# Optimization experiments

Hardware: AMD Instinct MI355X
Metric: run time of the kernel (lower is better)

The kernel has to match this reference:

```python
import jax, jax.numpy as jnp
import numpy as np


def setup_inputs() -> dict:
    key = jax.random.key(0)
    k1, k2 = jax.random.split(key)
    inputs = jax.random.normal(k1, (64, 16, 64, 512), dtype=jnp.float32)
    cluster_centers = jax.random.normal(k2, (64, 512), dtype=jnp.float32) * 0.05
    return {"inputs": inputs, "cluster_centers": cluster_centers}


def reference(inputs, cluster_centers):
    # inputs: (B, H, W, C); cluster_centers: (K, C)
    B, H, W, C = inputs.shape
    K = cluster_centers.shape[0]
    x = inputs.reshape(B, H * W, C)                      # (B, N, C)
    # soft assignments: softmax over K of x @ centers^T
    logits = jnp.einsum('bnc,kc->bnk', x, cluster_centers)
    a = jax.nn.softmax(logits, axis=-1)                  # (B, N, K)
    # VLAD rewritten to avoid (B,N,K,C) residual tensor:
    # sum_n a[b,n,k] * (x[b,n,:] - c[k,:])
    #   = (a^T @ x)[b,k,:] - (sum_n a[b,n,k]) * c[k,:]
    agg = jnp.einsum('bnk,bnc->bkc', a, x)               # (B, K, C)
    a_sum = jnp.sum(a, axis=1)                           # (B, K)
    vlad = agg - a_sum[:, :, None] * cluster_centers[None, :, :]
    vlad = vlad.reshape(B, K * C)
    # tf.nn.l2_normalize: x / sqrt(max(sum(x^2), eps)), eps=1e-12
    norm = jnp.sqrt(jnp.maximum(jnp.sum(vlad * vlad, axis=-1, keepdims=True), 1e-12))
    return vlad / norm
```

## Files before the change

kernel.cpp:

```cpp
#include <hip/hip_runtime.h>
#include <stdint.h>

#define NB 64
#define NN 1024
#define CDIM 512
#define KK 64

typedef __attribute__((ext_vector_type(4))) float f32x4;
typedef __attribute__((ext_vector_type(8))) short short8;

__device__ __forceinline__ unsigned short f2bf(float f) {
  unsigned int u = __float_as_uint(f);
  return (unsigned short)((u + 0x7fffu + ((u >> 16) & 1u)) >> 16);
}
__device__ __forceinline__ float bf2f(unsigned short h) {
  return __uint_as_float(((unsigned int)h) << 16);
}

__device__ __forceinline__ void lgkm_barrier() {
  asm volatile("s_waitcnt lgkmcnt(0)" ::: "memory");
  __builtin_amdgcn_sched_barrier(0);
  __builtin_amdgcn_s_barrier();
}

__global__ __launch_bounds__(256) void k0_cvt(const float* __restrict__ cc,
                                              unsigned short* __restrict__ ccb) {
  int i = blockIdx.x * 256 + threadIdx.x;
  ccb[i] = f2bf(cc[i]);
}

__global__ __launch_bounds__(256, 1) void k1_assign(const float* __restrict__ x,
    const unsigned short* __restrict__ ccb, unsigned int* __restrict__ a_t32,
    unsigned int* __restrict__ xT32) {
  const int b = blockIdx.y;
  const int tid = threadIdx.x;
  const int w = tid >> 6;
  const int l = tid & 63;
  const int lr = l & 15;
  const int lg = l >> 4;
  const int nc = (blockIdx.x << 2) + w;
  const int n0 = nc << 6;
  const int codd = l & 1;

  __shared__ unsigned int xsw_all[4][32 * 33];
  __shared__ unsigned int asw_all[4][64 * 33];
  unsigned int* xsw = xsw_all[w];
  unsigned int* asw = asw_all[w];

  const float* xr = x + ((size_t)b * NN + n0 + lr) * CDIM + (lg << 3);
  const unsigned short* cb = ccb + lr * CDIM + (lg << 3);
  const size_t xTbase = ((size_t)((b << 4) + nc)) << 14;
  const size_t atbase = ((size_t)((b << 4) + nc)) << 11;

  f32x4 acc[4][4];
  #pragma unroll
  for (int i = 0; i < 4; ++i)
    #pragma unroll
    for (int j = 0; j < 4; ++j) acc[i][j] = (f32x4){0.f, 0.f, 0.f, 0.f};

  #pragma unroll 2
  for (int step = 0; step < 16; ++step) {
    const int cs = step << 5;
    short8 af[4];
    #pragma unroll
    for (int tn = 0; tn < 4; ++tn) {
      f32x4 xa = *(const f32x4*)(xr + (size_t)(tn << 4) * CDIM + cs);
      f32x4 xb = *(const f32x4*)(xr + (size_t)(tn << 4) * CDIM + cs + 4);
      short8 t;
      t[0] = (short)f2bf(xa[0]); t[1] = (short)f2bf(xa[1]);
      t[2] = (short)f2bf(xa[2]); t[3] = (short)f2bf(xa[3]);
      t[4] = (short)f2bf(xb[0]); t[5] = (short)f2bf(xb[1]);
      t[6] = (short)f2bf(xb[2]); t[7] = (short)f2bf(xb[3]);
      af[tn] = t;
    }
    short8 bq0 = *(const short8*)(cb + cs);
    short8 bq1 = *(const short8*)(cb + 16 * CDIM + cs);
    short8 bq2 = *(const short8*)(cb + 32 * CDIM + cs);
    short8 bq3 = *(const short8*)(cb + 48 * CDIM + cs);
    #pragma unroll
    for (int tn = 0; tn < 4; ++tn) {
      acc[tn][0] = __builtin_amdgcn_mfma_f32_16x16x32_bf16(af[tn], bq0, acc[tn][0], 0, 0, 0);
      acc[tn][1] = __builtin_amdgcn_mfma_f32_16x16x32_bf16(af[tn], bq1, acc[tn][1], 0, 0, 0);
      acc[tn][2] = __builtin_amdgcn_mfma_f32_16x16x32_bf16(af[tn], bq2, acc[tn][2], 0, 0, 0);
      acc[tn][3] = __builtin_amdgcn_mfma_f32_16x16x32_bf16(af[tn], bq3, acc[tn][3], 0, 0, 0);
    }
    #pragma unroll
    for (int tn = 0; tn < 4; ++tn) {
      #pragma unroll
      for (int q = 0; q < 4; ++q) {
        unsigned int own = ((const unsigned int*)&af[tn])[q];
        unsigned int oth = (unsigned int)__shfl_xor((int)own, 1);
        unsigned int v = codd ? ((oth >> 16) | (own & 0xffff0000u))
                              : ((own & 0xffffu) | (oth << 16));
        xsw[((lg << 3) + (q << 1) + codd) * 33 + (tn << 3) + (lr >> 1)] = v;
      }
    }
    #pragma unroll
    for (int i = 0; i < 16; ++i) {
      const int row = (i << 1) + (l >> 5);
      xT32[xTbase + ((size_t)(cs + row) << 5) + (l & 31)] = xsw[row * 33 + (l & 31)];
    }
  }

  #pragma unroll
  for (int tn = 0; tn < 4; ++tn) {
    #pragma unroll
    for (int j = 0; j < 4; ++j) {
      float m = fmaxf(fmaxf(acc[tn][0][j], acc[tn][1][j]),
                      fmaxf(acc[tn][2][j], acc[tn][3][j]));
      m = fmaxf(m, __shfl_xor(m, 1));
      m = fmaxf(m, __shfl_xor(m, 2));
      m = fmaxf(m, __shfl_xor(m, 4));
      m = fmaxf(m, __shfl_xor(m, 8));
      float e0 = __expf(acc[tn][0][j] - m);
      float e1 = __expf(acc[tn][1][j] - m);
      float e2 = __expf(acc[tn][2][j] - m);
      float e3 = __expf(acc[tn][3][j] - m);
      float s = e0 + e1 + e2 + e3;
      s += __shfl_xor(s, 1); s += __shfl_xor(s, 2);
      s += __shfl_xor(s, 4); s += __shfl_xor(s, 8);
      float inv = 1.0f / s;
      acc[tn][0][j] = e0 * inv;
      acc[tn][1][j] = e1 * inv;
      acc[tn][2][j] = e2 * inv;
      acc[tn][3][j] = e3 * inv;
    }
  }
  #pragma unroll
  for (int tn = 0; tn < 4; ++tn)
    #pragma unroll
    for (int tk = 0; tk < 4; ++tk)
      #pragma unroll
      for (int jp = 0; jp < 2; ++jp) {
        unsigned int v = (unsigned int)f2bf(acc[tn][tk][2 * jp]) |
                         ((unsigned int)f2bf(acc[tn][tk][2 * jp + 1]) << 16);
        asw[((tk << 4) + lr) * 33 + (tn << 3) + (lg << 1) + jp] = v;
      }
  #pragma unroll
  for (int i = 0; i < 32; ++i) {
    const int k = (i << 1) + (l >> 5);
    a_t32[atbase + ((size_t)k << 5) + (l & 31)] = asw[k * 33 + (l & 31)];
  }
}

#define XRS 38
__global__ __launch_bounds__(256) void k2_agg(
    const unsigned short* __restrict__ a_t, const unsigned int* __restrict__ xT32,
    const float* __restrict__ cc, float* __restrict__ out,
    float* __restrict__ sumsq) {
  const int b = blockIdx.y;
  const int c0 = blockIdx.x << 6;
  const int tid = threadIdx.x;
  const int w = tid >> 6;
  const int l = tid & 63;
  const int lr = l & 15;
  const int lg = l >> 4;

  __shared__ unsigned int xs[2][64 * XRS];
  __shared__ float red[4];

  f32x4 acc[4];
  #pragma unroll
  for (int i = 0; i < 4; ++i) acc[i] = (f32x4){0.f, 0.f, 0.f, 0.f};
  float ssum = 0.f;

  const unsigned short* ap =
      a_t + (((size_t)(b << 4)) << 12) + (((w << 4) + lr) << 6) + (lg << 3);
  const unsigned int* xg =
      xT32 + (((size_t)(b << 4)) << 14) + ((c0 + (tid >> 5)) << 5) + (tid & 31);

  #pragma unroll
  for (int p = 0; p < 8; ++p) {
    const int f = (p << 8) + tid;
    xs[0][(f >> 5) * XRS + (f & 31)] = xg[p << 8];
  }
  short8 a_cur0 = *(const short8*)(ap);
  short8 a_cur1 = *(const short8*)(ap + 32);
  lgkm_barrier();

  for (int it = 0; it < 16; ++it) {
    const int cur = it & 1;
    unsigned int xr[8];
    short8 a_nxt0, a_nxt1;
    if (it < 15) {
      const size_t cho = ((size_t)(it + 1)) << 14;
      const size_t cha = ((size_t)(it + 1)) << 12;
      #pragma unroll
      for (int p = 0; p < 8; ++p) xr[p] = xg[cho + (p << 8)];
      a_nxt0 = *(const short8*)(ap + cha);
      a_nxt1 = *(const short8*)(ap + cha + 32);
    }
    #pragma unroll
    for (int i = 0; i < 8; ++i)
      ssum += bf2f((unsigned short)a_cur0[i]) + bf2f((unsigned short)a_cur1[i]);
    #pragma unroll
    for (int ns = 0; ns < 64; ns += 32) {
      const short8 af = ns == 0 ? a_cur0 : a_cur1;
      #pragma unroll
      for (int ct = 0; ct < 4; ++ct) {
        const int row = (ct << 4) + lr;
        const unsigned long long* bp = (const unsigned long long*)
            &xs[cur][row * XRS + (ns >> 1) + (lg << 2)];
        union { unsigned long long q[2]; short8 s; } u;
        u.q[0] = bp[0];
        u.q[1] = bp[1];
        acc[ct] = __builtin_amdgcn_mfma_f32_16x16x32_bf16(af, u.s, acc[ct], 0, 0, 0);
      }
    }
    if (it < 15) {
      #pragma unroll
      for (int p = 0; p < 8; ++p) {
        const int f = (p << 8) + tid;
        xs[cur ^ 1][(f >> 5) * XRS + (f & 31)] = xr[p];
      }
      a_cur0 = a_nxt0;
      a_cur1 = a_nxt1;
    }
    lgkm_barrier();
  }

  ssum += __shfl_xor(ssum, 16);
  ssum += __shfl_xor(ssum, 32);

  float lsum = 0.f;
  #pragma unroll
  for (int j = 0; j < 4; ++j) {
    const float asum_e = __shfl(ssum, (lg << 2) + j);
    #pragma unroll
    for (int ct = 0; ct < 4; ++ct) {
      int k = (w << 4) + (lg << 2) + j;
      int c = c0 + (ct << 4) + lr;
      float v = acc[ct][j] - asum_e * cc[k * CDIM + c];
      out[((size_t)b << 15) + (k << 9) + c] = v;
      lsum += v * v;
    }
  }
  lsum += __shfl_xor(lsum, 1);  lsum += __shfl_xor(lsum, 2);
  lsum += __shfl_xor(lsum, 4);  lsum += __shfl_xor(lsum, 8);
  lsum += __shfl_xor(lsum, 16); lsum += __shfl_xor(lsum, 32);
  if (l == 0) red[w] = lsum;
  __syncthreads();
  if (tid == 0) atomicAdd(&sumsq[b], red[0] + red[1] + red[2] + red[3]);
}

__global__ __launch_bounds__(256) void k3_norm(float* __restrict__ out,
                                               const float* __restrict__ sumsq) {
  int idx = blockIdx.x * 256 + threadIdx.x;
  int b = idx >> 13;
  float s = sumsq[b];
  float scale = 1.0f / sqrtf(fmaxf(s, 1e-12f));
  f32x4* io = (f32x4*)out;
  f32x4 v = io[idx];
  v[0] *= scale; v[1] *= scale; v[2] *= scale; v[3] *= scale;
  io[idx] = v;
}

extern "C" void kernel_launch(void* const* d_in, const int* in_sizes, int n_in,
                              void* d_out, int out_size, void* d_ws, size_t ws_size,
                              hipStream_t stream) {
  const float* x  = (const float*)d_in[0];
  const float* cc = (const float*)d_in[1];
  float* out = (float*)d_out;
  char* ws = (char*)d_ws;
  unsigned short* a_t = (unsigned short*)ws;
  unsigned int* a_t32 = (unsigned int*)ws;
  unsigned short* ccb = (unsigned short*)(ws + (8u << 20));
  float* sumsq = (float*)(ws + (8u << 20) + (64u << 10));
  unsigned int* xT32 = (unsigned int*)(ws + (16u << 20));

  (void)hipMemsetAsync(sumsq, 0, NB * 4, stream);
  k0_cvt<<<dim3((KK * CDIM) / 256), 256, 0, stream>>>(cc, ccb);
  k1_assign<<<dim3(4, NB), 256, 0, stream>>>(x, ccb, a_t32, xT32);
  k2_agg<<<dim3(8, NB), 256, 0, stream>>>(a_t, xT32, cc, out, sumsq);
  k3_norm<<<dim3(2048), 256, 0, stream>>>(out, sumsq);
}
```

Measured before the change: 79.03 us.

## Split assign kernel's channel reduction across wave pairs to double block count

Each 64-row chunk in k1_assign is now handled by two waves that each reduce over half of the channels. Partial logits are exchanged through shared memory, and each wave computes softmax for half of the row tiles. The grid doubles from 256 to 512 blocks and launch bounds allow two blocks per CU, giving more parallelism over the memory-bound load of x. In exchange the kernel adds a shared-memory exchange, two block barriers and more LDS use.

```diff
diff --git a/kernel.cpp b/kernel.cpp
--- a/kernel.cpp
+++ b/kernel.cpp
@@ -29,7 +29,7 @@
   ccb[i] = f2bf(cc[i]);
 }
 
-__global__ __launch_bounds__(256, 1) void k1_assign(const float* __restrict__ x,
+__global__ __launch_bounds__(256, 2) void k1_assign(const float* __restrict__ x,
     const unsigned short* __restrict__ ccb, unsigned int* __restrict__ a_t32,
     unsigned int* __restrict__ xT32) {
   const int b = blockIdx.y;
@@ -38,19 +38,23 @@
   const int l = tid & 63;
   const int lr = l & 15;
   const int lg = l >> 4;
-  const int nc = (blockIdx.x << 2) + w;
+  const int pair = w >> 1;
+  const int ch = w & 1;
+  const int nc = (blockIdx.x << 1) + pair;
   const int n0 = nc << 6;
+  const int cbase = ch << 8;
   const int codd = l & 1;
 
   __shared__ unsigned int xsw_all[4][32 * 33];
-  __shared__ unsigned int asw_all[4][64 * 33];
+  __shared__ unsigned int asw_all[2][64 * 33];
+  __shared__ f32x4 pacc[2][2][2][4][64];
+
   unsigned int* xsw = xsw_all[w];
-  unsigned int* asw = asw_all[w];
-
-  const float* xr = x + ((size_t)b * NN + n0 + lr) * CDIM + (lg << 3);
-  const unsigned short* cb = ccb + lr * CDIM + (lg << 3);
+  unsigned int* asw = asw_all[pair];
+
+  const float* xr = x + ((size_t)b * NN + n0 + lr) * CDIM + cbase + (lg << 3);
+  const unsigned short* cb = ccb + lr * CDIM + cbase + (lg << 3);
   const size_t xTbase = ((size_t)((b << 4) + nc)) << 14;
-  const size_t atbase = ((size_t)((b << 4) + nc)) << 11;
 
   f32x4 acc[4][4];
   #pragma unroll
@@ -59,7 +63,7 @@
     for (int j = 0; j < 4; ++j) acc[i][j] = (f32x4){0.f, 0.f, 0.f, 0.f};
 
   #pragma unroll 2
-  for (int step = 0; step < 16; ++step) {
+  for (int step = 0; step < 8; ++step) {
     const int cs = step << 5;
     short8 af[4];
     #pragma unroll
@@ -98,48 +102,84 @@
     #pragma unroll
     for (int i = 0; i < 16; ++i) {
       const int row = (i << 1) + (l >> 5);
-      xT32[xTbase + ((size_t)(cs + row) << 5) + (l & 31)] = xsw[row * 33 + (l & 31)];
-    }
-  }
-
-  #pragma unroll
-  for (int tn = 0; tn < 4; ++tn) {
-    #pragma unroll
-    for (int j = 0; j < 4; ++j) {
-      float m = fmaxf(fmaxf(acc[tn][0][j], acc[tn][1][j]),
-                      fmaxf(acc[tn][2][j], acc[tn][3][j]));
-      m = fmaxf(m, __shfl_xor(m, 1));
-      m = fmaxf(m, __shfl_xor(m, 2));
-      m = fmaxf(m, __shfl_xor(m, 4));
-      m = fmaxf(m, __shfl_xor(m, 8));
-      float e0 = __expf(acc[tn][0][j] - m);
-      float e1 = __expf(acc[tn][1][j] - m);
-      float e2 = __expf(acc[tn][2][j] - m);
-      float e3 = __expf(acc[tn][3][j] - m);
-      float s = e0 + e1 + e2 + e3;
-      s += __shfl_xor(s, 1); s += __shfl_xor(s, 2);
-      s += __shfl_xor(s, 4); s += __shfl_xor(s, 8);
-      float inv = 1.0f / s;
-      acc[tn][0][j] = e0 * inv;
-      acc[tn][1][j] = e1 * inv;
-      acc[tn][2][j] = e2 * inv;
-      acc[tn][3][j] = e3 * inv;
-    }
-  }
-  #pragma unroll
-  for (int tn = 0; tn < 4; ++tn)
-    #pragma unroll
-    for (int tk = 0; tk < 4; ++tk)
-      #pragma unroll
-      for (int jp = 0; jp < 2; ++jp) {
-        unsigned int v = (unsigned int)f2bf(acc[tn][tk][2 * jp]) |
-                         ((unsigned int)f2bf(acc[tn][tk][2 * jp + 1]) << 16);
-        asw[((tk << 4) + lr) * 33 + (tn << 3) + (lg << 1) + jp] = v;
-      }
-  #pragma unroll
-  for (int i = 0; i < 32; ++i) {
-    const int k = (i << 1) + (l >> 5);
-    a_t32[atbase + ((size_t)k << 5) + (l & 31)] = asw[k * 33 + (l & 31)];
+      xT32[xTbase + ((size_t)(cbase + cs + row) << 5) + (l & 31)] =
+          xsw[row * 33 + (l & 31)];
+    }
+  }
+
+  {
+    const int nd0 = ch ? 0 : 2;
+    #pragma unroll
+    for (int t2 = 0; t2 < 2; ++t2)
+      #pragma unroll
+      for (int tk = 0; tk < 4; ++tk)
+        pacc[pair][ch][t2][tk][l] = acc[nd0 + t2][tk];
+  }
+  __syncthreads();
+  {
+    const int d0 = ch ? 2 : 0;
+    #pragma unroll
+    for (int t2 = 0; t2 < 2; ++t2)
+      #pragma unroll
+      for (int tk = 0; tk < 4; ++tk) {
+        f32x4 o = pacc[pair][1 - ch][t2][tk][l];
+        acc[d0 + t2][0 + tk] += 0;
+        acc[d0 + t2][tk][0] += o[0];
+        acc[d0 + t2][tk][1] += o[1];
+        acc[d0 + t2][tk][2] += o[2];
+        acc[d0 + t2][tk][3] += o[3];
+      }
+  }
+
+  {
+    const int d0 = ch ? 2 : 0;
+    #pragma unroll
+    for (int t2 = 0; t2 < 2; ++t2) {
+      const int tn = d0 + t2;
+      #pragma unroll
+      for (int j = 0; j < 4; ++j) {
+        float m = fmaxf(fmaxf(acc[tn][0][j], acc[tn][1][j]),
+                        fmaxf(acc[tn][2][j], acc[tn][3][j]));
+        m = fmaxf(m, __shfl_xor(m, 1));
+        m = fmaxf(m, __shfl_xor(m, 2));
+        m = fmaxf(m, __shfl_xor(m, 4));
+        m = fmaxf(m, __shfl_xor(m, 8));
+        float e0 = __expf(acc[tn][0][j] - m);
+        float e1 = __expf(acc[tn][1][j] - m);
+        float e2 = __expf(acc[tn][2][j] - m);
+        float e3 = __expf(acc[tn][3][j] - m);
+        float s = e0 + e1 + e2 + e3;
+        s += __shfl_xor(s, 1); s += __shfl_xor(s, 2);
+        s += __shfl_xor(s, 4); s += __shfl_xor(s, 8);
+        float inv = 1.0f / s;
+        acc[tn][0][j] = e0 * inv;
+        acc[tn][1][j] = e1 * inv;
+        acc[tn][2][j] = e2 * inv;
+        acc[tn][3][j] = e3 * inv;
+      }
+      #pragma unroll
+      for (int tk = 0; tk < 4; ++tk)
+        #pragma unroll
+        for (int jp = 0; jp < 2; ++jp) {
+          unsigned int v = (unsigned int)f2bf(acc[tn][tk][2 * jp]) |
+                           ((unsigned int)f2bf(acc[tn][tk][2 * jp + 1]) << 16);
+          asw[((tk << 4) + lr) * 33 + (tn << 3) + (lg << 1) + jp] = v;
+        }
+    }
+  }
+  __syncthreads();
+
+  {
+    const size_t atb0 = ((size_t)((b << 4) + (blockIdx.x << 1))) << 11;
+    #pragma unroll
+    for (int i = 0; i < 16; ++i) {
+      const int f = (i << 8) + tid;
+      const int p = f >> 11;
+      const int k = (f >> 5) & 63;
+      const int col = f & 31;
+      a_t32[atb0 + (((size_t)p) << 11) + (k << 5) + col] =
+          asw_all[p][k * 33 + col];
+    }
   }
 }
 
@@ -270,7 +310,7 @@
 
   (void)hipMemsetAsync(sumsq, 0, NB * 4, stream);
   k0_cvt<<<dim3((KK * CDIM) / 256), 256, 0, stream>>>(cc, ccb);
-  k1_assign<<<dim3(4, NB), 256, 0, stream>>>(x, ccb, a_t32, xT32);
+  k1_assign<<<dim3(8, NB), 256, 0, stream>>>(x, ccb, a_t32, xT32);
   k2_agg<<<dim3(8, NB), 256, 0, stream>>>(a_t, xT32, cc, out, sumsq);
   k3_norm<<<dim3(2048), 256, 0, stream>>>(out, sumsq);
 }
```

New measurement: 108.0 us. 36.7% more time.
